# Kernel optimization log

Measured on AMD Instinct MI355X. Metric: run time of the kernel, lower is better.

The kernel has to match this reference:

```python
import jax, jax.numpy as jnp
import numpy as np

N_NODES = 4096
N_GRAPHS = 128
D_IN = 128
HEADS = 4
KEY_SIZE = 32  # == num_channels
D_OUT = 32 * D_IN  # num_channels * irreps.dim


def setup_inputs() -> dict:
    key = jax.random.key(0)
    ks = jax.random.split(key, 5)
    nodes = jax.random.normal(ks[0], (N_NODES, D_IN), dtype=jnp.float32)
    # 128 graphs of 32 nodes each, packed: sum(n_node) == N_NODES
    n_node = jnp.full((N_GRAPHS,), N_NODES // N_GRAPHS, dtype=jnp.int32)
    s_in = 1.0 / np.sqrt(D_IN)
    s_h = 1.0 / np.sqrt(HEADS * KEY_SIZE)
    Wq = jax.random.normal(ks[1], (D_IN, HEADS, KEY_SIZE), dtype=jnp.float32) * s_in
    Wk = jax.random.normal(ks[2], (D_IN, HEADS, KEY_SIZE), dtype=jnp.float32) * s_in
    Wv = jax.random.normal(ks[3], (D_IN, HEADS, KEY_SIZE), dtype=jnp.float32) * s_in
    Wo = jax.random.normal(ks[4], (HEADS * KEY_SIZE, D_OUT), dtype=jnp.float32) * s_h
    bq = jnp.zeros((HEADS, KEY_SIZE), dtype=jnp.float32)
    bk = jnp.zeros((HEADS, KEY_SIZE), dtype=jnp.float32)
    bv = jnp.zeros((HEADS, KEY_SIZE), dtype=jnp.float32)
    bo = jnp.zeros((D_OUT,), dtype=jnp.float32)
    return {"nodes": nodes, "n_node": n_node, "Wq": Wq, "bq": bq,
            "Wk": Wk, "bk": bk, "Wv": Wv, "bv": bv, "Wo": Wo, "bo": bo}


def reference(nodes, n_node, Wq, bq, Wk, bk, Wv, bv, Wo, bo):
    N = nodes.shape[0]
    G = n_node.shape[0]
    # segment id per packed node (get_segment_ids)
    seg = jnp.repeat(jnp.arange(G), n_node, total_repeat_length=N)
    # per-head projections: [N, H, K]
    q = jnp.einsum('nd,dhk->nhk', nodes, Wq) + bq
    k = jnp.einsum('nd,dhk->nhk', nodes, Wk) + bk
    v = jnp.einsum('nd,dhk->nhk', nodes, Wv) + bv
    # dense logits masked to block-diagonal per-graph blocks: [H, N, N]
    logits = jnp.einsum('nhk,mhk->hnm', q, k) / jnp.sqrt(jnp.float32(KEY_SIZE))
    mask = seg[:, None] == seg[None, :]  # [N, N]
    logits = jnp.where(mask[None, :, :], logits, jnp.float32(-1e30))
    attn = jax.nn.softmax(logits, axis=-1)
    out = jnp.einsum('hnm,mhk->nhk', attn, v).reshape(N, HEADS * KEY_SIZE)
    return out @ Wo + bo  # [N, num_channels * d_in]
```

## Files before the change

kernel.cpp:

```cpp
#include <hip/hip_runtime.h>
#include <hip/hip_bf16.h>


typedef __attribute__((ext_vector_type(4))) float f32x4;
typedef __attribute__((ext_vector_type(8))) short s16x8;
typedef __attribute__((ext_vector_type(4))) short s16x4;
typedef __attribute__((ext_vector_type(8))) __bf16 bf16x8;

static __device__ __forceinline__ short f2bf(float f) {
  union { float f; unsigned u; } v; v.f = f;
  unsigned r = v.u + 0x7fffu + ((v.u >> 16) & 1u);
  return (short)(r >> 16);
}

static __device__ __forceinline__ f32x4 mfma16(s16x8 a, s16x8 b, f32x4 c) {
  return __builtin_amdgcn_mfma_f32_16x16x32_bf16(
      __builtin_bit_cast(bf16x8, a), __builtin_bit_cast(bf16x8, b), c, 0, 0, 0);
}

__global__ __launch_bounds__(64) void k1_qkv_attn(
    const float* __restrict__ nodes,
    const float* __restrict__ Wq, const float* __restrict__ bq,
    const float* __restrict__ Wk, const float* __restrict__ bk,
    const float* __restrict__ Wv, const float* __restrict__ bv,
    unsigned short* __restrict__ attout)
{
  const int g = blockIdx.x;
  const int h = blockIdx.y;
  const int lane = threadIdx.x;
  const int l15 = lane & 15;
  const int qd = lane >> 4;

  __shared__ alignas(16) short sN[32][136];
  __shared__ alignas(16) short sQ[32][40];
  __shared__ alignas(16) short sK[32][40];
  __shared__ alignas(16) short sVT[32][40];
  __shared__ alignas(16) short sP[32][40];

  const float* ng = nodes + g * 32 * 128;
  #pragma unroll
  for (int i = 0; i < 16; ++i) {
    int f4  = i * 64 + lane;
    int row = f4 >> 5;
    int c4  = (f4 & 31) << 2;
    float4 v = *(const float4*)(ng + row * 128 + c4);
    s16x4 p;
    p[0] = f2bf(v.x); p[1] = f2bf(v.y); p[2] = f2bf(v.z); p[3] = f2bf(v.w);
    *(s16x4*)&sN[row][c4] = p;
  }
  __syncthreads();

  s16x8 afrag[2][4];
  #pragma unroll
  for (int mt = 0; mt < 2; ++mt)
    #pragma unroll
    for (int kk = 0; kk < 4; ++kk)
      afrag[mt][kk] = *(const s16x8*)&sN[mt * 16 + l15][kk * 32 + qd * 8];

  const float* Wm[3] = {Wq, Wk, Wv};
  const float* Bm[3] = {bq, bk, bv};

  #pragma unroll
  for (int m3 = 0; m3 < 3; ++m3) {
    f32x4 acc[2][2];
    f32x4 zero = {0.f, 0.f, 0.f, 0.f};
    acc[0][0] = zero; acc[0][1] = zero; acc[1][0] = zero; acc[1][1] = zero;
    const float* W = Wm[m3];
    #pragma unroll
    for (int kk = 0; kk < 4; ++kk) {
      s16x8 bfr[2];
      #pragma unroll
      for (int nt = 0; nt < 2; ++nt) {
        const float* src = W + (kk * 32 + qd * 8) * 128 + h * 32 + nt * 16 + l15;
        s16x8 e;
        #pragma unroll
        for (int j = 0; j < 8; ++j) e[j] = f2bf(src[j * 128]);
        bfr[nt] = e;
      }
      #pragma unroll
      for (int mt = 0; mt < 2; ++mt)
        #pragma unroll
        for (int nt = 0; nt < 2; ++nt)
          acc[mt][nt] = mfma16(afrag[mt][kk], bfr[nt], acc[mt][nt]);
    }
    float b0 = Bm[m3][h * 32 + l15];
    float b1 = Bm[m3][h * 32 + 16 + l15];
    #pragma unroll
    for (int mt = 0; mt < 2; ++mt)
      #pragma unroll
      for (int nt = 0; nt < 2; ++nt) {
        float bb = nt ? b1 : b0;
        #pragma unroll
        for (int r = 0; r < 4; ++r) {
          int m = mt * 16 + qd * 4 + r;
          int c = nt * 16 + l15;
          float val = acc[mt][nt][r] + bb;
          if (m3 == 0)      sQ[m][c]  = f2bf(val * 0.17677669529663687f);
          else if (m3 == 1) sK[m][c]  = f2bf(val);
          else              sVT[c][m] = f2bf(val);
        }
      }
  }
  __syncthreads();

  s16x8 qf[2], kf[2];
  #pragma unroll
  for (int mt = 0; mt < 2; ++mt) qf[mt] = *(const s16x8*)&sQ[mt * 16 + l15][qd * 8];
  #pragma unroll
  for (int nt = 0; nt < 2; ++nt) kf[nt] = *(const s16x8*)&sK[nt * 16 + l15][qd * 8];
  f32x4 sacc[2][2];
  {
    f32x4 zero = {0.f, 0.f, 0.f, 0.f};
    #pragma unroll
    for (int mt = 0; mt < 2; ++mt)
      #pragma unroll
      for (int nt = 0; nt < 2; ++nt)
        sacc[mt][nt] = mfma16(qf[mt], kf[nt], zero);
  }

  #pragma unroll
  for (int mt = 0; mt < 2; ++mt)
    #pragma unroll
    for (int r = 0; r < 4; ++r) {
      float a0 = sacc[mt][0][r], a1 = sacc[mt][1][r];
      float mx = fmaxf(a0, a1);
      mx = fmaxf(mx, __shfl_xor(mx, 1, 64));
      mx = fmaxf(mx, __shfl_xor(mx, 2, 64));
      mx = fmaxf(mx, __shfl_xor(mx, 4, 64));
      mx = fmaxf(mx, __shfl_xor(mx, 8, 64));
      float e0 = __expf(a0 - mx), e1 = __expf(a1 - mx);
      float s = e0 + e1;
      s += __shfl_xor(s, 1, 64);
      s += __shfl_xor(s, 2, 64);
      s += __shfl_xor(s, 4, 64);
      s += __shfl_xor(s, 8, 64);
      float inv = 1.0f / s;
      int m = mt * 16 + qd * 4 + r;
      sP[m][l15]      = f2bf(e0 * inv);
      sP[m][16 + l15] = f2bf(e1 * inv);
    }
  __syncthreads();

  s16x8 pf[2], vf[2];
  #pragma unroll
  for (int mt = 0; mt < 2; ++mt) pf[mt] = *(const s16x8*)&sP[mt * 16 + l15][qd * 8];
  #pragma unroll
  for (int nt = 0; nt < 2; ++nt) vf[nt] = *(const s16x8*)&sVT[nt * 16 + l15][qd * 8];
  f32x4 oacc[2][2];
  {
    f32x4 zero = {0.f, 0.f, 0.f, 0.f};
    #pragma unroll
    for (int mt = 0; mt < 2; ++mt)
      #pragma unroll
      for (int nt = 0; nt < 2; ++nt)
        oacc[mt][nt] = mfma16(pf[mt], vf[nt], zero);
  }
  unsigned short* ao = attout + (g * 32) * 128 + h * 32;
  #pragma unroll
  for (int mt = 0; mt < 2; ++mt)
    #pragma unroll
    for (int nt = 0; nt < 2; ++nt)
      #pragma unroll
      for (int r = 0; r < 4; ++r) {
        int m = mt * 16 + qd * 4 + r;
        int c = nt * 16 + l15;
        ao[m * 128 + c] = (unsigned short)f2bf(oacc[mt][nt][r]);
      }
}

__global__ __launch_bounds__(256) void k2_transpose(
    const float* __restrict__ Wo, unsigned short* __restrict__ WoT)
{
  int idx = blockIdx.x * 256 + threadIdx.x;
  int n = idx >> 7;
  int k = idx & 127;
  WoT[idx] = (unsigned short)f2bf(Wo[k * 4096 + n]);
}

__global__ __launch_bounds__(256) void k3_gemm(
    const unsigned short* __restrict__ A,
    const unsigned short* __restrict__ BT,
    const float* __restrict__ bo,
    float* __restrict__ C)
{
  __shared__ alignas(16) short sA[128][136];
  __shared__ alignas(16) short sB[128][136];
  const int t  = threadIdx.x;
  const int m0 = blockIdx.y << 7;
  const int n0 = blockIdx.x << 7;

  #pragma unroll
  for (int i = 0; i < 8; ++i) {
    int id  = i * 256 + t;
    int row = id >> 4;
    int ch  = (id & 15) << 3;
    *(s16x8*)&sA[row][ch] = *(const s16x8*)(A  + (m0 + row) * 128 + ch);
    *(s16x8*)&sB[row][ch] = *(const s16x8*)(BT + (n0 + row) * 128 + ch);
  }
  __syncthreads();

  const int w    = t >> 6;
  const int lane = t & 63;
  const int l15  = lane & 15;
  const int qd   = lane >> 4;
  const int wm   = (w >> 1) << 6;
  const int wn   = (w & 1) << 6;

  f32x4 acc[4][4];
  {
    f32x4 zero = {0.f, 0.f, 0.f, 0.f};
    #pragma unroll
    for (int i = 0; i < 4; ++i)
      #pragma unroll
      for (int j = 0; j < 4; ++j) acc[i][j] = zero;
  }

  #pragma unroll
  for (int kk = 0; kk < 4; ++kk) {
    s16x8 af[4], bf[4];
    #pragma unroll
    for (int i = 0; i < 4; ++i)
      af[i] = *(const s16x8*)&sA[wm + i * 16 + l15][kk * 32 + qd * 8];
    #pragma unroll
    for (int j = 0; j < 4; ++j)
      bf[j] = *(const s16x8*)&sB[wn + j * 16 + l15][kk * 32 + qd * 8];
    #pragma unroll
    for (int i = 0; i < 4; ++i)
      #pragma unroll
      for (int j = 0; j < 4; ++j)
        acc[i][j] = mfma16(af[i], bf[j], acc[i][j]);
  }

  float bov[4];
  #pragma unroll
  for (int j = 0; j < 4; ++j) bov[j] = bo[n0 + wn + j * 16 + l15];

  #pragma unroll
  for (int i = 0; i < 4; ++i) {
    int rbase = m0 + wm + i * 16 + qd * 4;
    #pragma unroll
    for (int r = 0; r < 4; ++r) {
      float* crow = C + (rbase + r) * 4096 + n0 + wn + l15;
      #pragma unroll
      for (int j = 0; j < 4; ++j)
        crow[j * 16] = acc[i][j][r] + bov[j];
    }
  }
}

extern "C" void kernel_launch(void* const* d_in, const int* in_sizes, int n_in,
                              void* d_out, int out_size, void* d_ws, size_t ws_size,
                              hipStream_t stream) {
  const float* nodes = (const float*)d_in[0];
  const float* Wq = (const float*)d_in[2];
  const float* bq = (const float*)d_in[3];
  const float* Wk = (const float*)d_in[4];
  const float* bk = (const float*)d_in[5];
  const float* Wv = (const float*)d_in[6];
  const float* bv = (const float*)d_in[7];
  const float* Wo = (const float*)d_in[8];
  const float* bo = (const float*)d_in[9];
  float* out = (float*)d_out;

  unsigned short* attout = (unsigned short*)d_ws;
  unsigned short* WoT    = attout + 4096 * 128;

  k1_qkv_attn<<<dim3(128, 4), 64, 0, stream>>>(nodes, Wq, bq, Wk, bk, Wv, bv, attout);
  k2_transpose<<<2048, 256, 0, stream>>>(Wo, WoT);
  k3_gemm<<<dim3(32, 32), 256, 0, stream>>>(attout, WoT, bo, out);
}
```

Baseline: 116.6 us.

## Pretranspose QKV and Wo weights to bf16 in one LDS-tiled prep kernel

Adds a prep kernel that converts Wq/Wk/Wv/Wo to bf16 and transposes them through shared memory, reading rows with coalesced float4 loads and writing 16-byte stores. It replaces the per-element strided Wo transpose kernel. The attention kernel now loads its QKV weight fragments as 16-byte vector loads from the pre-transposed buffer, instead of doing eight scalar strided fp32 loads and conversions per fragment in each of the 512 blocks. The cost is a serial dependency on the prep kernel, which runs on only 70 blocks, and a larger workspace.

```diff
diff --git a/kernel.cpp b/kernel.cpp
--- a/kernel.cpp
+++ b/kernel.cpp
@@ -18,11 +18,43 @@
       __builtin_bit_cast(bf16x8, a), __builtin_bit_cast(bf16x8, b), c, 0, 0, 0);
 }
 
+__global__ __launch_bounds__(256) void k0_prep(
+    const float* __restrict__ Wq, const float* __restrict__ Wk,
+    const float* __restrict__ Wv, const float* __restrict__ Wo,
+    unsigned short* __restrict__ WqkvT, unsigned short* __restrict__ WoT)
+{
+  __shared__ alignas(16) short sT[64][136];
+  const int b = blockIdx.x;
+  const float* in; unsigned short* out; int C; int n0;
+  if (b < 64)      { in = Wo; out = WoT;           C = 4096; n0 = b << 6; }
+  else if (b < 66) { in = Wq; out = WqkvT;         C = 128;  n0 = (b - 64) << 6; }
+  else if (b < 68) { in = Wk; out = WqkvT + 16384; C = 128;  n0 = (b - 66) << 6; }
+  else             { in = Wv; out = WqkvT + 32768; C = 128;  n0 = (b - 68) << 6; }
+  const int t  = threadIdx.x;
+  const int rr = t >> 4;
+  const int c4 = (t & 15) << 2;
+  #pragma unroll
+  for (int i = 0; i < 8; ++i) {
+    int r = i * 16 + rr;
+    float4 v = *(const float4*)(in + r * C + n0 + c4);
+    sT[c4 + 0][r] = f2bf(v.x);
+    sT[c4 + 1][r] = f2bf(v.y);
+    sT[c4 + 2][r] = f2bf(v.z);
+    sT[c4 + 3][r] = f2bf(v.w);
+  }
+  __syncthreads();
+  const int c  = t >> 2;
+  const int k0 = (t & 3) << 5;
+  #pragma unroll
+  for (int j = 0; j < 4; ++j)
+    *(s16x8*)&out[(n0 + c) * 128 + k0 + j * 8] = *(const s16x8*)&sT[c][k0 + j * 8];
+}
+
 __global__ __launch_bounds__(64) void k1_qkv_attn(
     const float* __restrict__ nodes,
-    const float* __restrict__ Wq, const float* __restrict__ bq,
-    const float* __restrict__ Wk, const float* __restrict__ bk,
-    const float* __restrict__ Wv, const float* __restrict__ bv,
+    const unsigned short* __restrict__ WqkvT,
+    const float* __restrict__ bq, const float* __restrict__ bk,
+    const float* __restrict__ bv,
     unsigned short* __restrict__ attout)
 {
   const int g = blockIdx.x;
@@ -57,32 +89,27 @@
     for (int kk = 0; kk < 4; ++kk)
       afrag[mt][kk] = *(const s16x8*)&sN[mt * 16 + l15][kk * 32 + qd * 8];
 
-  const float* Wm[3] = {Wq, Wk, Wv};
   const float* Bm[3] = {bq, bk, bv};
 
   #pragma unroll
   for (int m3 = 0; m3 < 3; ++m3) {
+    const unsigned short* WT = WqkvT + m3 * 16384;
+    s16x8 bfr[4][2];
+    #pragma unroll
+    for (int kk = 0; kk < 4; ++kk)
+      #pragma unroll
+      for (int nt = 0; nt < 2; ++nt)
+        bfr[kk][nt] = *(const s16x8*)&WT[(h * 32 + nt * 16 + l15) * 128 + kk * 32 + qd * 8];
     f32x4 acc[2][2];
     f32x4 zero = {0.f, 0.f, 0.f, 0.f};
     acc[0][0] = zero; acc[0][1] = zero; acc[1][0] = zero; acc[1][1] = zero;
-    const float* W = Wm[m3];
-    #pragma unroll
-    for (int kk = 0; kk < 4; ++kk) {
-      s16x8 bfr[2];
-      #pragma unroll
-      for (int nt = 0; nt < 2; ++nt) {
-        const float* src = W + (kk * 32 + qd * 8) * 128 + h * 32 + nt * 16 + l15;
-        s16x8 e;
-        #pragma unroll
-        for (int j = 0; j < 8; ++j) e[j] = f2bf(src[j * 128]);
-        bfr[nt] = e;
-      }
+    #pragma unroll
+    for (int kk = 0; kk < 4; ++kk)
       #pragma unroll
       for (int mt = 0; mt < 2; ++mt)
         #pragma unroll
         for (int nt = 0; nt < 2; ++nt)
-          acc[mt][nt] = mfma16(afrag[mt][kk], bfr[nt], acc[mt][nt]);
-    }
+          acc[mt][nt] = mfma16(afrag[mt][kk], bfr[kk][nt], acc[mt][nt]);
     float b0 = Bm[m3][h * 32 + l15];
     float b1 = Bm[m3][h * 32 + 16 + l15];
     #pragma unroll
@@ -168,15 +195,6 @@
       }
 }
 
-__global__ __launch_bounds__(256) void k2_transpose(
-    const float* __restrict__ Wo, unsigned short* __restrict__ WoT)
-{
-  int idx = blockIdx.x * 256 + threadIdx.x;
-  int n = idx >> 7;
-  int k = idx & 127;
-  WoT[idx] = (unsigned short)f2bf(Wo[k * 4096 + n]);
-}
-
 __global__ __launch_bounds__(256) void k3_gemm(
     const unsigned short* __restrict__ A,
     const unsigned short* __restrict__ BT,
@@ -264,8 +282,9 @@
 
   unsigned short* attout = (unsigned short*)d_ws;
   unsigned short* WoT    = attout + 4096 * 128;
-
-  k1_qkv_attn<<<dim3(128, 4), 64, 0, stream>>>(nodes, Wq, bq, Wk, bk, Wv, bv, attout);
-  k2_transpose<<<2048, 256, 0, stream>>>(Wo, WoT);
+  unsigned short* WqkvT  = WoT + 4096 * 128;
+
+  k0_prep<<<70, 256, 0, stream>>>(Wq, Wk, Wv, Wo, WqkvT, WoT);
+  k1_qkv_attn<<<dim3(128, 4), 64, 0, stream>>>(nodes, WqkvT, bq, bk, bv, attout);
   k3_gemm<<<dim3(32, 32), 256, 0, stream>>>(attout, WoT, bo, out);
 }
```

Result: faster. 109.2 us (-6.4%).
